# Optimization experiments

Measured on AMD Instinct MI355X. Metric: run time of the kernel, lower is better.

The kernel has to match this reference:

```python
import jax, jax.numpy as jnp
import numpy as np
import math

TOPK = 32

def setup_inputs() -> dict:
    key = jax.random.key(0)
    k1, k2, k3, k4 = jax.random.split(key, 4)
    B, D_e, D_o, T, H, W = 2, 128, 256, 16, 64, 64
    H_ref = W_ref = 32  # resolution_ref = 2
    THW_ref = T * H_ref * W_ref
    HW_ref = H_ref * W_ref
    return {
        "m_in": jax.random.normal(k1, (B, D_e, T, H, W), jnp.float32),
        "m_out": jax.random.normal(k2, (B, D_o, T, H, W), jnp.float32),
        "q_in": jax.random.normal(k3, (B, D_e, H, W), jnp.float32),
        "qk_ref": jax.random.normal(k4, (B, THW_ref, HW_ref), jnp.float32),
    }


def reference(m_in, m_out, q_in, qk_ref):
    B, D_e, T, H, W = m_in.shape
    D_o = m_out.shape[1]
    _, THW_ref, HW_ref = qk_ref.shape
    res = int(math.sqrt(H * W // HW_ref))
    H_ref, W_ref = H // res, W // res
    s = res
    k = TOPK

    # top-k memory blocks for each of the HW_ref query blocks
    topk_val, topk_idx = jax.lax.top_k(jnp.swapaxes(qk_ref, 1, 2), k)  # [B, HW_ref, k]
    # torch path scatters one-hot then uses nonzero -> gather order is ascending-index;
    # softmax-attention over n is permutation invariant, but sort for exact faithfulness.
    idx_sorted = jnp.sort(topk_idx, axis=-1)

    def blockify(m, D):
        # [B,D,T,H,W] -> [B, T*H_ref*W_ref, s, s, D]
        m = m.reshape(B, D, T, H_ref, s, W_ref, s)
        m = m.transpose(0, 2, 3, 5, 4, 6, 1)  # B,T,H_ref,W_ref,s,s,D
        return m.reshape(B, T * H_ref * W_ref, s, s, D)

    m_in_b = blockify(m_in, D_e)
    m_out_b = blockify(m_out, D_o)

    flat_idx = idx_sorted.reshape(B, HW_ref * k)
    gather = jax.vmap(lambda mb, i: mb[i])  # per-batch fancy gather of blocks
    m_in_sel = gather(m_in_b, flat_idx).reshape(B, H_ref, W_ref, k * s * s, D_e)
    m_out_sel = gather(m_out_b, flat_idx).reshape(B, H_ref, W_ref, k * s * s, D_o)

    # query blocks: [B, H_ref, W_ref, D_e, s, s]
    q = q_in.reshape(B, D_e, H_ref, s, W_ref, s).transpose(0, 2, 4, 1, 3, 5)

    p = jnp.einsum('bhwnc,bhwcij->bhwijn', m_in_sel, q) / math.sqrt(D_e)
    p = jax.nn.softmax(p, axis=-1)
    mem_out = jnp.einsum('bhwnc,bhwijn->bchiwj', m_out_sel, p).reshape(B, D_o, H, W)

    kk = max(k // 4, 1)
    return mem_out, topk_idx[:, :, :kk], topk_val[:, :, :kk]
```

## Files before the change

### kernel.cpp

```cpp
#include <hip/hip_runtime.h>
#include <math.h>



__device__ inline unsigned mono_u32(float f) {
    unsigned b = __float_as_uint(f);
    return (b & 0x80000000u) ? ~b : (b | 0x80000000u);
}

__global__ __launch_bounds__(256) void qk_chunk_max(const float* __restrict__ qk,
                                                    float* __restrict__ Mx) {
    int wg = blockIdx.x;
    int cg = wg & 3;
    int chunk = (wg >> 2) & 63;
    int b = wg >> 8;
    int col = cg * 256 + threadIdx.x;
    const float* p = qk + ((size_t)b * 16384 + (size_t)chunk * 256) * 1024 + col;
    float m = -__builtin_inff();
#pragma unroll
    for (int rb = 0; rb < 16; ++rb) {
        float vv[16];
#pragma unroll
        for (int u = 0; u < 16; ++u)
            vv[u] = p[(size_t)(rb * 16 + u) * 1024];
#pragma unroll
        for (int u = 0; u < 16; ++u) m = fmaxf(m, vv[u]);
    }
    Mx[((size_t)b * 1024 + col) * 64 + chunk] = m;
}

__global__ __launch_bounds__(256) void qk_thresh(const float* __restrict__ Mx,
                                                 unsigned* __restrict__ t_u,
                                                 int* __restrict__ cnt) {
    int g = blockIdx.x * 256 + threadIdx.x;
    if (g < 2048) cnt[g] = 0;
    int colg = blockIdx.x * 4 + (threadIdx.x >> 6);
    int lane = threadIdx.x & 63;
    float mv = Mx[(size_t)colg * 64 + lane];
    unsigned long long key = ((unsigned long long)mono_u32(mv) << 32) | (unsigned)lane;
    int rank = 0;
#pragma unroll 8
    for (int j = 0; j < 64; ++j) {
        unsigned long long other = __shfl(key, j, 64);
        rank += (other > key) ? 1 : 0;
    }
    if (rank == 31) t_u[colg] = (unsigned)(key >> 32);
}

__global__ __launch_bounds__(256) void qk_filter(const float* __restrict__ qk,
                                                 const unsigned* __restrict__ t_u,
                                                 int* __restrict__ cnt,
                                                 unsigned long long* __restrict__ cand) {
    int wg = blockIdx.x;
    int cg = wg & 3;
    int chunk = (wg >> 2) & 63;
    int b = wg >> 8;
    int col = cg * 256 + threadIdx.x;
    int colg = b * 1024 + col;
    unsigned t = t_u[colg];
    const float* p = qk + ((size_t)b * 16384 + (size_t)chunk * 256) * 1024 + col;
    int n0 = chunk * 256;
#pragma unroll
    for (int rb = 0; rb < 16; ++rb) {
        float vv[16];
#pragma unroll
        for (int u = 0; u < 16; ++u)
            vv[u] = p[(size_t)(rb * 16 + u) * 1024];
#pragma unroll
        for (int u = 0; u < 16; ++u) {
            unsigned uu = mono_u32(vv[u]);
            if (uu >= t) {
                int pos = atomicAdd(&cnt[colg], 1);
                if (pos < 256) {
                    int gi = n0 + rb * 16 + u;
                    cand[(size_t)colg * 256 + pos] =
                        ((unsigned long long)uu << 32) |
                        (unsigned long long)(16383 - gi);
                }
            }
        }
    }
}

__global__ __launch_bounds__(256) void topk_select(const unsigned long long* __restrict__ cand,
                                                   const int* __restrict__ cnt,
                                                   const float* __restrict__ qk,
                                                   float* __restrict__ out_idx,
                                                   float* __restrict__ out_val,
                                                   int* __restrict__ idx_sorted) {
    int bid = blockIdx.x;
    int tid = threadIdx.x;
    __shared__ unsigned long long sc[256];
    __shared__ unsigned long long selk[32];

    int C = cnt[bid];
    if (C <= 256) {
        if (tid < C) sc[tid] = cand[(size_t)bid * 256 + tid];
        __syncthreads();
        if (tid < C) {
            unsigned long long mine = sc[tid];
            int rank = 0;
            for (int j = 0; j < C; ++j) rank += (sc[j] > mine) ? 1 : 0;
            if (rank < 32) selk[rank] = mine;
        }
        __syncthreads();
    } else {
        int b = bid >> 10, q = bid & 1023;
        const float* colp = qk + (size_t)b * 16384 * 1024 + q;
        unsigned long long prev = ~0ull;
#pragma unroll 1
        for (int s = 0; s < 32; ++s) {
            unsigned long long best = 0;
            for (int r = tid; r < 16384; r += 256) {
                unsigned long long k =
                    ((unsigned long long)mono_u32(colp[(size_t)r * 1024]) << 32) |
                    (unsigned long long)(16383 - r);
                if (k < prev && k > best) best = k;
            }
            sc[tid] = best;
            __syncthreads();
            for (int off = 128; off >= 1; off >>= 1) {
                if (tid < off && sc[tid + off] > sc[tid]) sc[tid] = sc[tid + off];
                __syncthreads();
            }
            if (tid == 0) selk[s] = sc[0];
            __syncthreads();
            prev = selk[s];
        }
    }

    if (tid < 8) {
        unsigned long long k = selk[tid];
        unsigned uv = (unsigned)(k >> 32);
        unsigned bits = (uv & 0x80000000u) ? (uv ^ 0x80000000u) : ~uv;
        out_val[(size_t)bid * 8 + tid] = __uint_as_float(bits);
        int gi = 16383 - (int)(k & 0xFFFFFFFFull);
        out_idx[(size_t)bid * 8 + tid] = (float)gi;
    }
    if (tid < 32) {
        int mine = 16383 - (int)(selk[tid] & 0xFFFFFFFFull);
        int rank = 0;
#pragma unroll
        for (int j = 0; j < 32; ++j) {
            int oj = 16383 - (int)(selk[j] & 0xFFFFFFFFull);
            rank += (oj < mine) ? 1 : 0;
        }
        idx_sorted[(size_t)bid * 32 + rank] = mine;
    }
}

template <int D, int T>
__global__ __launch_bounds__(256) void blockify_tiled(const float* __restrict__ in,
                                                      float* __restrict__ out) {
    constexpr int NCH = D / 64;
    int wg = blockIdx.x;
    int ch = wg % NCH;
    int hb = (wg / NCH) % 32;
    int t  = (wg / (NCH * 32)) % T;
    int b  = wg / (NCH * 32 * T);
    int c0 = ch * 64;
    int tid = threadIdx.x;

    __shared__ float tile[64][129];

    {
        int x = tid & 63;
        int rw = tid >> 6;
#pragma unroll 8
        for (int i = 0; i < 32; ++i) {
            int r = i * 4 + rw;
            int c = r >> 1, si = r & 1;
            tile[c][si * 64 + x] =
                in[((((size_t)b * D + c0 + c) * T + t) * 64 + (2 * hb + si)) * 64 + x];
        }
    }
    __syncthreads();

    {
        int p = tid >> 6;
        int cc = tid & 63;
        int si = p >> 1, sj = p & 1;
        size_t nbase = (((size_t)b * T + t) * 1024 + (size_t)hb * 32);
#pragma unroll 8
        for (int wb = 0; wb < 32; ++wb) {
            out[(nbase + wb) * 4 * D + (size_t)p * D + c0 + cc] =
                tile[cc][si * 64 + 2 * wb + sj];
        }
    }
}

__global__ __launch_bounds__(256) void attn_kernel(const float* __restrict__ m_in_b,
                                                   const float* __restrict__ m_out_b,
                                                   const float* __restrict__ q_b,
                                                   const int* __restrict__ idx_sorted,
                                                   float* __restrict__ out) {
    int bid = blockIdx.x;
    int b = bid >> 10, qblk = bid & 1023;
    int hb = qblk >> 5, wb = qblk & 31;
    int tid = threadIdx.x;
    int w = tid >> 6, lane = tid & 63;

    __shared__ float K[64][129];
    __shared__ float Q[4][128];
    __shared__ float P[4][128];
    __shared__ int   blks[32];

    if (tid < 32) blks[tid] = idx_sorted[(size_t)bid * 32 + tid];
    {
        const float* qsrc = q_b + (size_t)bid * 512;
        ((float*)Q)[tid]       = qsrc[tid];
        ((float*)Q)[tid + 256] = qsrc[tid + 256];
    }
    __syncthreads();

    const float scale = 0.08838834764831845f;
    float s01[2];
#pragma unroll 1
    for (int half = 0; half < 2; ++half) {
        if (half) __syncthreads();
#pragma unroll 4
        for (int ki = 0; ki < 16; ++ki) {
            int blk = blks[half * 16 + ki];
            const float* src = m_in_b + ((size_t)b * 16384 + blk) * 512;
            int p0 = tid >> 7, c0 = tid & 127;
            K[ki * 4 + p0][c0]     = src[tid];
            K[ki * 4 + p0 + 2][c0] = src[tid + 256];
        }
        __syncthreads();
        float acc = 0.f;
#pragma unroll 4
        for (int c = 0; c < 128; ++c) acc += K[lane][c] * Q[w][c];
        s01[half] = acc * scale;
    }

    float m = fmaxf(s01[0], s01[1]);
#pragma unroll
    for (int off = 32; off >= 1; off >>= 1) m = fmaxf(m, __shfl_xor(m, off, 64));
    float e0 = expf(s01[0] - m), e1 = expf(s01[1] - m);
    float sum = e0 + e1;
#pragma unroll
    for (int off = 32; off >= 1; off >>= 1) sum += __shfl_xor(sum, off, 64);
    float inv = 1.0f / sum;
    P[w][lane]      = e0 * inv;
    P[w][lane + 64] = e1 * inv;
    __syncthreads();

    float a0 = 0.f, a1 = 0.f, a2 = 0.f, a3 = 0.f;
    int d = tid;
#pragma unroll 1
    for (int ki = 0; ki < 32; ++ki) {
        const float* vsrc = m_out_b + ((size_t)b * 16384 + blks[ki]) * 1024;
#pragma unroll
        for (int p = 0; p < 4; ++p) {
            float vv = vsrc[p * 256 + d];
            int n = ki * 4 + p;
            a0 += P[0][n] * vv; a1 += P[1][n] * vv;
            a2 += P[2][n] * vv; a3 += P[3][n] * vv;
        }
    }
    size_t base = (((size_t)b * 256 + d) * 64 + hb * 2) * 64 + wb * 2;
    out[base]      = a0;
    out[base + 1]  = a1;
    out[base + 64] = a2;
    out[base + 65] = a3;
}

extern "C" void kernel_launch(void* const* d_in, const int* in_sizes, int n_in,
                              void* d_out, int out_size, void* d_ws, size_t ws_size,
                              hipStream_t stream) {
    const float* m_in  = (const float*)d_in[0];
    const float* m_out = (const float*)d_in[1];
    const float* q_in  = (const float*)d_in[2];
    const float* qk    = (const float*)d_in[3];

    char* ws = (char*)d_ws;
    float* m_out_b = (float*)(ws);
    float* m_in_b  = (float*)(ws + 134217728);
    float* q_b     = (float*)(ws + 201326592);
    int*   idxs    = (int*)  (ws + 205520896);

    unsigned long long* cand = (unsigned long long*)(ws);
    float*    Mx  = (float*)   (ws + 4194304);
    unsigned* t_u = (unsigned*)(ws + 4718592);
    int*      cnt = (int*)     (ws + 4726784);

    float* out     = (float*)d_out;
    float* out_mem = out;
    float* out_idx = out + 2097152;
    float* out_val = out + 2113536;

    qk_chunk_max<<<512, 256, 0, stream>>>(qk, Mx);
    qk_thresh   <<<512, 256, 0, stream>>>(Mx, t_u, cnt);
    qk_filter   <<<512, 256, 0, stream>>>(qk, t_u, cnt, cand);
    topk_select <<<2048, 256, 0, stream>>>(cand, cnt, qk, out_idx, out_val, idxs);

    blockify_tiled<128, 16><<<2 * 16 * 32 * 2, 256, 0, stream>>>(m_in, m_in_b);
    blockify_tiled<128, 1><<<2 * 1 * 32 * 2, 256, 0, stream>>>(q_in, q_b);
    blockify_tiled<256, 16><<<2 * 16 * 32 * 4, 256, 0, stream>>>(m_out, m_out_b);
    attn_kernel<<<2048, 256, 0, stream>>>(m_in_b, m_out_b, q_b, idxs, out_mem);
}
```

Measured before the change: 473.2 us.

## Vectorize top-k scans with float4 and rework blockify transpose with swizzled tiles

The qk chunk-max and filter kernels now read four columns per thread with float4 loads over 128-row chunks, which doubles the number of chunk maxima to 128. The threshold kernel ranks two keys per lane to pick the 32nd largest of those 128 maxima. The blockify transposes use a 128x128 XOR-swizzled shared tile with float4 global loads and stores in place of scalar padded-tile accesses. The intent is better memory coalescing and fewer memory transactions. The cost is fewer workgroups and more register pressure in the filter kernel, and the finer chunks give a tighter threshold.

```diff
diff --git a/kernel.cpp b/kernel.cpp
--- a/kernel.cpp
+++ b/kernel.cpp
@@ -11,22 +11,25 @@
 __global__ __launch_bounds__(256) void qk_chunk_max(const float* __restrict__ qk,
                                                     float* __restrict__ Mx) {
     int wg = blockIdx.x;
-    int cg = wg & 3;
-    int chunk = (wg >> 2) & 63;
-    int b = wg >> 8;
-    int col = cg * 256 + threadIdx.x;
-    const float* p = qk + ((size_t)b * 16384 + (size_t)chunk * 256) * 1024 + col;
-    float m = -__builtin_inff();
+    int chunk = wg & 127;
+    int b = wg >> 7;
+    int tid = threadIdx.x;
+    const float4* p = (const float4*)(qk + ((size_t)b * 16384 + (size_t)chunk * 128) * 1024) + tid;
+    float4 m4;
+    m4.x = m4.y = m4.z = m4.w = -__builtin_inff();
 #pragma unroll
     for (int rb = 0; rb < 16; ++rb) {
-        float vv[16];
-#pragma unroll
-        for (int u = 0; u < 16; ++u)
-            vv[u] = p[(size_t)(rb * 16 + u) * 1024];
-#pragma unroll
-        for (int u = 0; u < 16; ++u) m = fmaxf(m, vv[u]);
-    }
-    Mx[((size_t)b * 1024 + col) * 64 + chunk] = m;
+        float4 v[8];
+#pragma unroll
+        for (int u = 0; u < 8; ++u)
+            v[u] = p[(size_t)(rb * 8 + u) * 256];
+#pragma unroll
+        for (int u = 0; u < 8; ++u) {
+            m4.x = fmaxf(m4.x, v[u].x); m4.y = fmaxf(m4.y, v[u].y);
+            m4.z = fmaxf(m4.z, v[u].z); m4.w = fmaxf(m4.w, v[u].w);
+        }
+    }
+    ((float4*)Mx)[(size_t)wg * 256 + tid] = m4;
 }
 
 __global__ __launch_bounds__(256) void qk_thresh(const float* __restrict__ Mx,
@@ -36,15 +39,22 @@
     if (g < 2048) cnt[g] = 0;
     int colg = blockIdx.x * 4 + (threadIdx.x >> 6);
     int lane = threadIdx.x & 63;
-    float mv = Mx[(size_t)colg * 64 + lane];
-    unsigned long long key = ((unsigned long long)mono_u32(mv) << 32) | (unsigned)lane;
-    int rank = 0;
+    int b = colg >> 10, col = colg & 1023;
+    const float* base = Mx + (size_t)b * 131072 + col;
+    float v0 = base[(size_t)lane * 1024];
+    float v1 = base[(size_t)(lane + 64) * 1024];
+    unsigned long long k0 = ((unsigned long long)mono_u32(v0) << 32) | (unsigned)lane;
+    unsigned long long k1 = ((unsigned long long)mono_u32(v1) << 32) | (unsigned)(lane + 64);
+    int r0 = 0, r1 = 0;
 #pragma unroll 8
     for (int j = 0; j < 64; ++j) {
-        unsigned long long other = __shfl(key, j, 64);
-        rank += (other > key) ? 1 : 0;
-    }
-    if (rank == 31) t_u[colg] = (unsigned)(key >> 32);
+        unsigned long long o0 = __shfl(k0, j, 64);
+        unsigned long long o1 = __shfl(k1, j, 64);
+        r0 += (o0 > k0) ? 1 : 0; r0 += (o1 > k0) ? 1 : 0;
+        r1 += (o0 > k1) ? 1 : 0; r1 += (o1 > k1) ? 1 : 0;
+    }
+    if (r0 == 31) t_u[colg] = (unsigned)(k0 >> 32);
+    if (r1 == 31) t_u[colg] = (unsigned)(k1 >> 32);
 }
 
 __global__ __launch_bounds__(256) void qk_filter(const float* __restrict__ qk,
@@ -52,31 +62,42 @@
                                                  int* __restrict__ cnt,
                                                  unsigned long long* __restrict__ cand) {
     int wg = blockIdx.x;
-    int cg = wg & 3;
-    int chunk = (wg >> 2) & 63;
-    int b = wg >> 8;
-    int col = cg * 256 + threadIdx.x;
-    int colg = b * 1024 + col;
-    unsigned t = t_u[colg];
-    const float* p = qk + ((size_t)b * 16384 + (size_t)chunk * 256) * 1024 + col;
-    int n0 = chunk * 256;
+    int chunk = wg & 127;
+    int b = wg >> 7;
+    int tid = threadIdx.x;
+    const float4* p = (const float4*)(qk + ((size_t)b * 16384 + (size_t)chunk * 128) * 1024) + tid;
+    uint4 tu = ((const uint4*)t_u)[b * 256 + tid];
+    int colg0 = b * 1024 + 4 * tid;
 #pragma unroll
     for (int rb = 0; rb < 16; ++rb) {
-        float vv[16];
-#pragma unroll
-        for (int u = 0; u < 16; ++u)
-            vv[u] = p[(size_t)(rb * 16 + u) * 1024];
-#pragma unroll
-        for (int u = 0; u < 16; ++u) {
-            unsigned uu = mono_u32(vv[u]);
-            if (uu >= t) {
-                int pos = atomicAdd(&cnt[colg], 1);
-                if (pos < 256) {
-                    int gi = n0 + rb * 16 + u;
-                    cand[(size_t)colg * 256 + pos] =
-                        ((unsigned long long)uu << 32) |
-                        (unsigned long long)(16383 - gi);
-                }
+        float4 v[8];
+#pragma unroll
+        for (int u = 0; u < 8; ++u)
+            v[u] = p[(size_t)(rb * 8 + u) * 256];
+#pragma unroll
+        for (int u = 0; u < 8; ++u) {
+            int row = chunk * 128 + rb * 8 + u;
+            unsigned ux = mono_u32(v[u].x), uy = mono_u32(v[u].y);
+            unsigned uz = mono_u32(v[u].z), uw = mono_u32(v[u].w);
+            if (ux >= tu.x) {
+                int pos = atomicAdd(&cnt[colg0 + 0], 1);
+                if (pos < 256) cand[(size_t)(colg0 + 0) * 256 + pos] =
+                    ((unsigned long long)ux << 32) | (unsigned long long)(16383 - row);
+            }
+            if (uy >= tu.y) {
+                int pos = atomicAdd(&cnt[colg0 + 1], 1);
+                if (pos < 256) cand[(size_t)(colg0 + 1) * 256 + pos] =
+                    ((unsigned long long)uy << 32) | (unsigned long long)(16383 - row);
+            }
+            if (uz >= tu.z) {
+                int pos = atomicAdd(&cnt[colg0 + 2], 1);
+                if (pos < 256) cand[(size_t)(colg0 + 2) * 256 + pos] =
+                    ((unsigned long long)uz << 32) | (unsigned long long)(16383 - row);
+            }
+            if (uw >= tu.w) {
+                int pos = atomicAdd(&cnt[colg0 + 3], 1);
+                if (pos < 256) cand[(size_t)(colg0 + 3) * 256 + pos] =
+                    ((unsigned long long)uw << 32) | (unsigned long long)(16383 - row);
             }
         }
     }
@@ -150,41 +171,54 @@
 }
 
 template <int D, int T>
-__global__ __launch_bounds__(256) void blockify_tiled(const float* __restrict__ in,
-                                                      float* __restrict__ out) {
-    constexpr int NCH = D / 64;
+__global__ __launch_bounds__(256) void blockify2(const float* __restrict__ in,
+                                                 float* __restrict__ out) {
+    constexpr int NH = D / 128;
+    __shared__ float tile[128][128];
     int wg = blockIdx.x;
-    int ch = wg % NCH;
-    int hb = (wg / NCH) % 32;
-    int t  = (wg / (NCH * 32)) % T;
-    int b  = wg / (NCH * 32 * T);
-    int c0 = ch * 64;
-    int tid = threadIdx.x;
-
-    __shared__ float tile[64][129];
+    int h  = wg % NH;
+    int hb = (wg / NH) % 32;
+    int t  = (wg / (NH * 32)) % T;
+    int b  = wg / (NH * 32 * T);
+    int tid = threadIdx.x;
 
     {
-        int x = tid & 63;
-        int rw = tid >> 6;
-#pragma unroll 8
-        for (int i = 0; i < 32; ++i) {
-            int r = i * 4 + rw;
-            int c = r >> 1, si = r & 1;
-            tile[c][si * 64 + x] =
-                in[((((size_t)b * D + c0 + c) * T + t) * 64 + (2 * hb + si)) * 64 + x];
+        int m   = tid & 31;
+        int cl0 = tid >> 5;
+        float4 v[16];
+#pragma unroll
+        for (int pass = 0; pass < 16; ++pass) {
+            int c = pass * 8 + cl0;
+            const float* src = in +
+                ((size_t)(b * D + h * 128 + c) * T + t) * 4096 + (size_t)hb * 128;
+            v[pass] = *(const float4*)(src + 4 * m);
+        }
+#pragma unroll
+        for (int pass = 0; pass < 16; ++pass) {
+            int c = pass * 8 + cl0;
+            int sw = ((c >> 2) & 31) << 2;
+            *(float4*)&tile[c][(4 * m) ^ sw] = v[pass];
         }
     }
     __syncthreads();
 
     {
-        int p = tid >> 6;
-        int cc = tid & 63;
-        int si = p >> 1, sj = p & 1;
-        size_t nbase = (((size_t)b * T + t) * 1024 + (size_t)hb * 32);
-#pragma unroll 8
-        for (int wb = 0; wb < 32; ++wb) {
-            out[(nbase + wb) * 4 * D + (size_t)p * D + c0 + cc] =
-                tile[cc][si * 64 + 2 * wb + sj];
+        size_t slab = (((size_t)b * T + t) * 1024 + (size_t)hb * 32) * (4 * D) +
+                      (size_t)h * 128;
+#pragma unroll
+        for (int it = 0; it < 16; ++it) {
+            int flat = it * 1024 + tid * 4;
+            int cl = flat & 127;
+            int pp = (flat >> 7) & 3;
+            int wb = flat >> 9;
+            int pos = ((pp >> 1) << 6) + 2 * wb + (pp & 1);
+            int sw = ((cl >> 2) & 31) << 2;
+            float4 o;
+            o.x = tile[cl + 0][pos ^ sw];
+            o.y = tile[cl + 1][pos ^ sw];
+            o.z = tile[cl + 2][pos ^ sw];
+            o.w = tile[cl + 3][pos ^ sw];
+            *(float4*)(out + slab + (size_t)wb * 4 * D + (size_t)pp * D + cl) = o;
         }
     }
 }
@@ -281,21 +315,21 @@
 
     unsigned long long* cand = (unsigned long long*)(ws);
     float*    Mx  = (float*)   (ws + 4194304);
-    unsigned* t_u = (unsigned*)(ws + 4718592);
-    int*      cnt = (int*)     (ws + 4726784);
+    unsigned* t_u = (unsigned*)(ws + 5242880);
+    int*      cnt = (int*)     (ws + 5251072);
 
     float* out     = (float*)d_out;
     float* out_mem = out;
     float* out_idx = out + 2097152;
     float* out_val = out + 2113536;
 
-    qk_chunk_max<<<512, 256, 0, stream>>>(qk, Mx);
+    qk_chunk_max<<<256, 256, 0, stream>>>(qk, Mx);
     qk_thresh   <<<512, 256, 0, stream>>>(Mx, t_u, cnt);
-    qk_filter   <<<512, 256, 0, stream>>>(qk, t_u, cnt, cand);
+    qk_filter   <<<256, 256, 0, stream>>>(qk, t_u, cnt, cand);
     topk_select <<<2048, 256, 0, stream>>>(cand, cnt, qk, out_idx, out_val, idxs);
 
-    blockify_tiled<128, 16><<<2 * 16 * 32 * 2, 256, 0, stream>>>(m_in, m_in_b);
-    blockify_tiled<128, 1><<<2 * 1 * 32 * 2, 256, 0, stream>>>(q_in, q_b);
-    blockify_tiled<256, 16><<<2 * 16 * 32 * 4, 256, 0, stream>>>(m_out, m_out_b);
+    blockify2<128, 16><<<1024, 256, 0, stream>>>(m_in, m_in_b);
+    blockify2<128, 1><<<64, 256, 0, stream>>>(q_in, q_b);
+    blockify2<256, 16><<<2048, 256, 0, stream>>>(m_out, m_out_b);
     attn_kernel<<<2048, 256, 0, stream>>>(m_in_b, m_out_b, q_b, idxs, out_mem);
 }
```

After: 542.6 us. +14.7%, slower.
